# Performance work log

Measured on AMD Instinct MI355X. Metric: run time of the kernel, lower is better.

## Reference

```python
import jax, jax.numpy as jnp
import numpy as np

B, N, D, H, DH = 2, 2048, 1024, 16, 64
INNER = H * DH          # 1024
FF_INNER = 4 * D        # 4096 (GEGLU)
EPS = 1e-5


def setup_inputs() -> dict:
    key = jax.random.key(0)
    ks = jax.random.split(key, 12)
    s = D ** -0.5
    return {
        "x": jax.random.normal(ks[0], (B, N, D), jnp.float32),
        "Wq": jax.random.normal(ks[1], (D, INNER), jnp.float32) * s,
        "Wk": jax.random.normal(ks[2], (D, INNER), jnp.float32) * s,
        "Wv": jax.random.normal(ks[3], (D, INNER), jnp.float32) * s,
        "Wo": jax.random.normal(ks[4], (INNER, D), jnp.float32) * s,
        "bo": jnp.zeros((D,), jnp.float32),
        "ln1_g": jnp.ones((D,), jnp.float32),
        "ln1_b": jnp.zeros((D,), jnp.float32),
        "ln3_g": jnp.ones((D,), jnp.float32),
        "ln3_b": jnp.zeros((D,), jnp.float32),
        "Wff1": jax.random.normal(ks[5], (D, 2 * FF_INNER), jnp.float32) * s,
        "bff1": jnp.zeros((2 * FF_INNER,), jnp.float32),
        "Wff2": jax.random.normal(ks[6], (FF_INNER, D), jnp.float32) * (FF_INNER ** -0.5),
        "bff2": jnp.zeros((D,), jnp.float32),
    }


def _layernorm(x, g, b):
    mu = jnp.mean(x, axis=-1, keepdims=True)
    var = jnp.mean(jnp.square(x - mu), axis=-1, keepdims=True)
    return (x - mu) * jax.lax.rsqrt(var + EPS) * g + b


def reference(x, Wq, Wk, Wv, Wo, bo, ln1_g, ln1_b, ln3_g, ln3_b, Wff1, bff1, Wff2, bff2):
    scale = DH ** -0.5

    # norm1 + self-attention (attn1)
    x_features = _layernorm(x, ln1_g, ln1_b)
    q = (x_features @ Wq).reshape(B, N, H, DH)
    k = (x_features @ Wk).reshape(B, N, H, DH)
    v = (x_features @ Wv).reshape(B, N, H, DH)
    sim = jnp.einsum('bihd,bjhd->bhij', q, k) * scale      # (B,H,N,N) full scores
    attn = jax.nn.softmax(sim, axis=-1)
    inter_out = jnp.einsum('bhij,bjhd->bhid', attn, v)     # (B,H,N,DH)
    out = inter_out.transpose(0, 2, 1, 3).reshape(B, N, INNER)
    attended_x = out @ Wo + bo
    x = attended_x + x

    # norm3 + GEGLU feed-forward
    h = _layernorm(x, ln3_g, ln3_b) @ Wff1 + bff1
    a, gate = h[..., :FF_INNER], h[..., FF_INNER:]
    x = (a * jax.nn.gelu(gate, approximate=False)) @ Wff2 + bff2 + x

    # match torch return: q,k,v as (b h) n d, attn = inter_out (b h n d)
    q_bh = q.transpose(0, 2, 1, 3).reshape(B * H, N, DH)
    k_bh = k.transpose(0, 2, 1, 3).reshape(B * H, N, DH)
    v_bh = v.transpose(0, 2, 1, 3).reshape(B * H, N, DH)
    return (x, q_bh, k_bh, v_bh, inter_out, x_features)
```

## Files before the change

kernel.cpp:

```cpp
#include <hip/hip_runtime.h>
#include <hip/hip_bf16.h>

#define B_ 2
#define N_ 2048
#define D_ 1024
#define H_ 16
#define DH_ 64
#define M_ 4096
#define FFI_ 4096

typedef __attribute__((ext_vector_type(8))) short bh8;
typedef __attribute__((ext_vector_type(4))) float f4;

#define DEV static __device__ __forceinline__

DEV short f2bf(float f) { __hip_bfloat16 h = __float2bfloat16(f); return *reinterpret_cast<short*>(&h); }
DEV float bf2f(short s) { __hip_bfloat16 h = *reinterpret_cast<__hip_bfloat16*>(&s); return __bfloat162float(h); }

#define GLDS(gp, lp) __builtin_amdgcn_global_load_lds((const __attribute__((address_space(1))) void*)(gp), (__attribute__((address_space(3))) void*)(lp), 16, 0, 0)
#define MFMA16(a,b,c) __builtin_amdgcn_mfma_f32_16x16x32_bf16(a,b,c,0,0,0)

__global__ __launch_bounds__(256) void ln_kernel(const float* __restrict__ x,
    const float* __restrict__ g, const float* __restrict__ b,
    float* __restrict__ outF, short* __restrict__ outB)
{
  const int row = blockIdx.x;
  const int t = threadIdx.x;
  const float4 v = reinterpret_cast<const float4*>(x + (long)row*D_)[t];
  float s = v.x+v.y+v.z+v.w;
  float sq = v.x*v.x+v.y*v.y+v.z*v.z+v.w*v.w;
  #pragma unroll
  for (int o=32;o>0;o>>=1){ s += __shfl_xor(s,o); sq += __shfl_xor(sq,o); }
  __shared__ float red[8];
  const int w = t>>6, l = t&63;
  if (l==0){ red[w]=s; red[4+w]=sq; }
  __syncthreads();
  s  = red[0]+red[1]+red[2]+red[3];
  sq = red[4]+red[5]+red[6]+red[7];
  const float mu = s*(1.f/D_);
  const float rstd = rsqrtf(sq*(1.f/D_) - mu*mu + 1e-5f);
  const float4 gv = reinterpret_cast<const float4*>(g)[t];
  const float4 bv = reinterpret_cast<const float4*>(b)[t];
  float4 y;
  y.x=(v.x-mu)*rstd*gv.x+bv.x; y.y=(v.y-mu)*rstd*gv.y+bv.y;
  y.z=(v.z-mu)*rstd*gv.z+bv.z; y.w=(v.w-mu)*rstd*gv.w+bv.w;
  if (outF) reinterpret_cast<float4*>(outF + (long)row*D_)[t] = y;
  short4 ys; ys.x=f2bf(y.x); ys.y=f2bf(y.y); ys.z=f2bf(y.z); ys.w=f2bf(y.w);
  reinterpret_cast<short4*>(outB + (long)row*D_)[t] = ys;
}

__global__ __launch_bounds__(256) void transpose_cast(const float* __restrict__ in,
    short* __restrict__ out, int R, int C)
{
  __shared__ float tile[32][33];
  const int tx = threadIdx.x & 31, ty = threadIdx.x >> 5;
  const int c0 = blockIdx.x*32, r0 = blockIdx.y*32;
  #pragma unroll
  for (int i=0;i<4;i++) tile[ty+i*8][tx] = in[(long)(r0+ty+i*8)*C + c0+tx];
  __syncthreads();
  #pragma unroll
  for (int i=0;i<4;i++) out[(long)(c0+ty+i*8)*R + r0+tx] = f2bf(tile[tx][ty+i*8]);
}

__global__ __launch_bounds__(256) void transpose_cast4(
    const float* __restrict__ i0, const float* __restrict__ i1,
    const float* __restrict__ i2, const float* __restrict__ i3,
    short* __restrict__ o0, short* __restrict__ o1,
    short* __restrict__ o2, short* __restrict__ o3)
{
  const int z = blockIdx.z;
  const float* in = z==0?i0 : z==1?i1 : z==2?i2 : i3;
  short* out      = z==0?o0 : z==1?o1 : z==2?o2 : o3;
  __shared__ float tile[32][33];
  const int tx = threadIdx.x & 31, ty = threadIdx.x >> 5;
  const int c0 = blockIdx.x*32, r0 = blockIdx.y*32;
  #pragma unroll
  for (int i=0;i<4;i++) tile[ty+i*8][tx] = in[(long)(r0+ty+i*8)*1024 + c0+tx];
  __syncthreads();
  #pragma unroll
  for (int i=0;i<4;i++) out[(long)(c0+ty+i*8)*1024 + r0+tx] = f2bf(tile[tx][ty+i*8]);
}

template<int BM>
DEV void gemm_core(const short* __restrict__ A, const short* __restrict__ BT, int K,
                   int m0, int n0, short* lA, short* lB, f4 (&acc)[BM/32][4])
{
  const int t = threadIdx.x, w = t>>6, l = t&63;
  const int wrow = (w>>1)*(BM/2), wcol = (w&1)*64;
  const int lr = l&15, lk = (l>>4)*8;
  const int sr = t>>2, sc = (t&3)*8;
  const short* gA = A  + (long)(m0+sr)*K + sc;
  const short* gB = BT + (long)(n0+sr)*K + sc;
  #pragma unroll
  for (int i=0;i<BM/32;i++)
    #pragma unroll
    for (int j=0;j<4;j++) acc[i][j] = f4{0.f,0.f,0.f,0.f};
  for (int k0=0; k0<K; k0+=32) {
    __syncthreads();
    #pragma unroll
    for (int i=0;i<BM/64;i++)
      GLDS(gA + (long)i*64*K, &lA[i*2048 + w*512]);
    GLDS(gB,              &lB[w*512]);
    GLDS(gB + (long)64*K, &lB[2048 + w*512]);
    gA += 32; gB += 32;
    asm volatile("s_waitcnt vmcnt(0)" ::: "memory");
    __syncthreads();
    bh8 af[BM/32], bf_[4];
    #pragma unroll
    for (int i=0;i<BM/32;i++) af[i] = *reinterpret_cast<const bh8*>(&lA[(wrow+i*16+lr)*32 + lk]);
    #pragma unroll
    for (int j=0;j<4;j++) bf_[j] = *reinterpret_cast<const bh8*>(&lB[(wcol+j*16+lr)*32 + lk]);
    #pragma unroll
    for (int i=0;i<BM/32;i++)
      #pragma unroll
      for (int j=0;j<4;j++)
        acc[i][j] = MFMA16(af[i], bf_[j], acc[i][j]);
  }
}

__global__ __launch_bounds__(256) void gemm_qkv(const short* __restrict__ A,
    const short* __restrict__ BTq, const short* __restrict__ BTk, const short* __restrict__ BTv,
    float* __restrict__ oQ, float* __restrict__ oK, float* __restrict__ oV,
    short* __restrict__ bQ, short* __restrict__ bK, short* __restrict__ bV)
{
  __shared__ short lA[4096], lB[4096];
  const int m0 = blockIdx.x*128;
  const int by = blockIdx.y, sel = by>>3, n0 = (by&7)*128;
  const short* BT = sel==0 ? BTq : (sel==1 ? BTk : BTv);
  float* oF = sel==0 ? oQ : (sel==1 ? oK : oV);
  short* oB = sel==0 ? bQ : (sel==1 ? bK : bV);
  const float bscale = sel==0 ? 0.125f : 1.0f;
  f4 acc[4][4];
  gemm_core<128>(A, BT, 1024, m0, n0, lA, lB, acc);
  const int t = threadIdx.x, w = t>>6, l = t&63;
  const int wrow=(w>>1)*64, wcol=(w&1)*64, lr=l&15;
  #pragma unroll
  for (int i=0;i<4;i++)
    #pragma unroll
    for (int j=0;j<4;j++)
      #pragma unroll
      for (int r=0;r<4;r++) {
        const int grow = m0 + wrow + i*16 + (l>>4)*4 + r;
        const int gcol = n0 + wcol + j*16 + lr;
        const int bb = grow >> 11, nn = grow & 2047;
        const int hh = gcol >> 6, dd = gcol & 63;
        const long oi = ((long)(bb*H_ + hh)*N_ + nn)*DH_ + dd;
        const float v = acc[i][j][r];
        oF[oi] = v;
        oB[oi] = f2bf(v * bscale);
      }
}

template<int MODE, int BM>
__global__ __launch_bounds__(256) void gemm_bt(const short* __restrict__ A,
    const short* __restrict__ BT, int Ndim, int K,
    const float* __restrict__ bias, const float* __restrict__ resid,
    float* __restrict__ outF, short* __restrict__ outB)
{
  __shared__ short lA[BM*32], lB[4096];
  const int m0 = blockIdx.x*BM, n0 = blockIdx.y*128;
  f4 acc[BM/32][4];
  gemm_core<BM>(A, BT, K, m0, n0, lA, lB, acc);
  const int t = threadIdx.x, w=t>>6, l=t&63;
  const int wrow=(w>>1)*(BM/2), wcol=(w&1)*64, lr=l&15;
  #pragma unroll
  for (int i=0;i<BM/32;i++)
    #pragma unroll
    for (int j=0;j<4;j++)
      #pragma unroll
      for (int r=0;r<4;r++) {
        const int grow = m0 + wrow + i*16 + (l>>4)*4 + r;
        const int gcol = n0 + wcol + j*16 + lr;
        const long oi = (long)grow*Ndim + gcol;
        const float v = acc[i][j][r] + bias[gcol];
        if (MODE==1) outF[oi] = v + resid[oi];
        else         outB[oi] = f2bf(v);
      }
}

__global__ __launch_bounds__(256) void attn_kernel(const short* __restrict__ Q,
    const short* __restrict__ Kb, const short* __restrict__ Vb,
    float* __restrict__ interOut, short* __restrict__ attnB)
{
  __shared__ short Kt[2*64*64];
  __shared__ short Vt[2*64*64];
  __shared__ short Pt[4*16*72];
  const int t = threadIdx.x, w = t>>6, l = t&63;
  const int bid = blockIdx.x;
  const int nb = (bid & 7)*128 + (bid >> 3);
  const int bh = nb >> 5;
  const int q0 = (nb & 31)*64;
  const int lr = l&15, lk = (l>>4)*8, g = l>>4;
  const long base = (long)bh * (N_*DH_);
  const int qrow = q0 + w*16;
  bh8 qf0 = *reinterpret_cast<const bh8*>(&Q[base + (long)(qrow+lr)*DH_ + lk]);
  bh8 qf1 = *reinterpret_cast<const bh8*>(&Q[base + (long)(qrow+lr)*DH_ + 32 + lk]);
  f4 o[4];
  #pragma unroll
  for (int i=0;i<4;i++) o[i]=f4{0.f,0.f,0.f,0.f};
  float m_run[4], l_run[4];
  #pragma unroll
  for (int r=0;r<4;r++){ m_run[r]=-1e30f; l_run[r]=0.f; }
  short* Pw = &Pt[w*16*72];
  const char* ldsK = (const char*)Kt;
  const int beta0 = w*2048 + l*16;
  const int srow = t>>3, sdp = t&7, sd = sdp*8;
  const int NT = N_/64;
  int4 vv[2];
  {
    const char* Kg = (const char*)(Kb + base);
    #pragma unroll
    for (int i=0;i<2;i++) {
      const int beta = beta0 + i*1024;
      const int krow = beta>>7, kpch = (beta>>4)&7;
      GLDS(Kg + krow*128 + (kpch ^ (krow&7))*16, (char*)Kt + (w*2+i)*1024);
    }
    #pragma unroll
    for (int it=0; it<2; it++)
      vv[it] = *reinterpret_cast<const int4*>(&Vb[base + (long)(it*32+srow)*DH_ + sd]);
  }
  for (int kt=0; kt<NT; kt++) {
    const int b = kt & 1;
    asm volatile("s_waitcnt vmcnt(0)" ::: "memory");
    #pragma unroll
    for (int it=0; it<2; it++) {
      const short* vs = reinterpret_cast<const short*>(&vv[it]);
      const int cb0 = (it*4 + (srow>>3)) ^ sdp;
      const int jc  = srow & 7;
      #pragma unroll
      for (int e=0;e<8;e++)
        Vt[b*4096 + (sd+e)*64 + ((cb0^e)<<3) + jc] = vs[e];
    }
    if (kt+1 < NT) {
      const char* Kg = (const char*)(Kb + base + (long)(kt+1)*64*DH_);
      #pragma unroll
      for (int i=0;i<2;i++) {
        const int beta = beta0 + i*1024;
        const int krow = beta>>7, kpch = (beta>>4)&7;
        GLDS(Kg + krow*128 + (kpch ^ (krow&7))*16, (char*)Kt + (b^1)*8192 + (w*2+i)*1024);
      }
      #pragma unroll
      for (int it=0; it<2; it++)
        vv[it] = *reinterpret_cast<const int4*>(&Vb[base + (long)((kt+1)*64 + it*32+srow)*DH_ + sd]);
    }
    asm volatile("s_waitcnt lgkmcnt(0)" ::: "memory");
    __builtin_amdgcn_s_barrier();
    f4 s[4];
    __builtin_amdgcn_s_setprio(1);
    #pragma unroll
    for (int cb=0;cb<4;cb++) {
      const int krow = cb*16+lr;
      const char* kr = ldsK + b*8192 + krow*128;
      bh8 kf0 = *reinterpret_cast<const bh8*>(kr + ((g  )^(lr&7))*16);
      bh8 kf1 = *reinterpret_cast<const bh8*>(kr + ((g+4)^(lr&7))*16);
      f4 z = f4{0.f,0.f,0.f,0.f};
      z = MFMA16(qf0, kf0, z);
      z = MFMA16(qf1, kf1, z);
      s[cb] = z;
    }
    __builtin_amdgcn_s_setprio(0);
    float mx[4];
    #pragma unroll
    for (int r=0;r<4;r++) mx[r] = fmaxf(fmaxf(s[0][r],s[1][r]), fmaxf(s[2][r],s[3][r]));
    #pragma unroll
    for (int mk=1; mk<16; mk<<=1)
      #pragma unroll
      for (int r=0;r<4;r++) mx[r] = fmaxf(mx[r], __shfl_xor(mx[r], mk));
    float rs[4];
    #pragma unroll
    for (int r=0;r<4;r++) {
      const float mn = fmaxf(m_run[r], mx[r]);
      const float al = __expf(m_run[r]-mn);
      m_run[r] = mn;
      l_run[r] *= al;
      float sum = 0.f;
      #pragma unroll
      for (int cb=0;cb<4;cb++) {
        const float pv = __expf(s[cb][r]-mn);
        sum += pv;
        Pw[((l>>4)*4 + r)*72 + cb*16 + lr] = f2bf(pv);
      }
      rs[r] = sum;
      #pragma unroll
      for (int cb=0;cb<4;cb++) o[cb][r] *= al;
    }
    #pragma unroll
    for (int mk=1; mk<16; mk<<=1)
      #pragma unroll
      for (int r=0;r<4;r++) rs[r] += __shfl_xor(rs[r], mk);
    #pragma unroll
    for (int r=0;r<4;r++) l_run[r] += rs[r];
    asm volatile("s_waitcnt lgkmcnt(0)" ::: "memory");
    __builtin_amdgcn_sched_barrier(0);
    bh8 pa0 = *reinterpret_cast<const bh8*>(&Pw[lr*72 + lk]);
    bh8 pa1 = *reinterpret_cast<const bh8*>(&Pw[lr*72 + 32 + lk]);
    #pragma unroll
    for (int kk=0; kk<2; kk++) {
      const bh8 pa = kk ? pa1 : pa0;
      __builtin_amdgcn_s_setprio(1);
      #pragma unroll
      for (int db=0; db<4; db++) {
        const int dd = db*16 + lr;
        const int ch = (kk*4 + g) ^ (dd&7) ^ ((dd>>3)&7);
        bh8 vf = *reinterpret_cast<const bh8*>(&Vt[b*4096 + dd*64 + ch*8]);
        o[db] = MFMA16(pa, vf, o[db]);
      }
      __builtin_amdgcn_s_setprio(0);
    }
    __builtin_amdgcn_s_barrier();
  }
  const int bb = bh>>4, hh = bh&15;
  #pragma unroll
  for (int db=0; db<4; db++)
    #pragma unroll
    for (int r=0;r<4;r++) {
      const int n = qrow + (l>>4)*4 + r;
      const int d = db*16 + lr;
      const float v = o[db][r] / l_run[r];
      interOut[base + (long)n*DH_ + d] = v;
      attnB[(long)(bb*N_ + n)*1024 + hh*DH_ + d] = f2bf(v);
    }
}

__global__ __launch_bounds__(256) void gelu_mul(const short* __restrict__ h, short* __restrict__ g)
{
  const long i = ((long)blockIdx.x*256 + threadIdx.x)*8;
  const long m = i >> 12;
  const int j = (int)(i & 4095);
  bh8 av = *reinterpret_cast<const bh8*>(&h[m*8192 + j]);
  bh8 gv = *reinterpret_cast<const bh8*>(&h[m*8192 + 4096 + j]);
  bh8 ov;
  #pragma unroll
  for (int e=0;e<8;e++) {
    const float a  = bf2f(av[e]);
    const float xg = bf2f(gv[e]);
    const float ge = 0.5f*xg*(1.f + erff(xg*0.70710678118f));
    ov[e] = f2bf(a*ge);
  }
  *reinterpret_cast<bh8*>(&g[i]) = ov;
}

extern "C" void kernel_launch(void* const* d_in, const int* in_sizes, int n_in,
                              void* d_out, int out_size, void* d_ws, size_t ws_size,
                              hipStream_t stream)
{
  const float* x    = (const float*)d_in[0];
  const float* Wq   = (const float*)d_in[1];
  const float* Wk   = (const float*)d_in[2];
  const float* Wv   = (const float*)d_in[3];
  const float* Wo   = (const float*)d_in[4];
  const float* bo   = (const float*)d_in[5];
  const float* ln1g = (const float*)d_in[6];
  const float* ln1b = (const float*)d_in[7];
  const float* ln3g = (const float*)d_in[8];
  const float* ln3b = (const float*)d_in[9];
  const float* Wff1 = (const float*)d_in[10];
  const float* bff1 = (const float*)d_in[11];
  const float* Wff2 = (const float*)d_in[12];
  const float* bff2 = (const float*)d_in[13];
  float* out = (float*)d_out;
  const long SZ = (long)M_*D_;
  float* out_x     = out;
  float* out_q     = out + SZ;
  float* out_k     = out + 2*SZ;
  float* out_v     = out + 3*SZ;
  float* out_inter = out + 4*SZ;
  float* out_xf    = out + 5*SZ;

  char* p = (char*)d_ws;
  auto alloc = [&](size_t bytes){ void* r = (void*)p; p += (bytes + 255) & ~(size_t)255; return r; };
  short* xf_bf  = (short*)alloc(SZ*2);
  short* q_bf   = (short*)alloc(SZ*2);
  short* k_bf   = (short*)alloc(SZ*2);
  short* v_bf   = (short*)alloc(SZ*2);
  short* at_bf  = (short*)alloc(SZ*2);
  float* x2     = (float*)alloc(SZ*4);
  short* x2n_bf = (short*)alloc(SZ*2);
  short* h_bf   = (short*)alloc((size_t)M_*8192*2);
  short* g_bf   = (short*)alloc((size_t)M_*4096*2);
  short* WqT    = (short*)alloc((size_t)1024*1024*2);
  short* WkT    = (short*)alloc((size_t)1024*1024*2);
  short* WvT    = (short*)alloc((size_t)1024*1024*2);
  short* WoT    = (short*)alloc((size_t)1024*1024*2);
  short* Wff1T  = (short*)alloc((size_t)8192*1024*2);
  short* Wff2T  = (short*)alloc((size_t)1024*4096*2);
  (void)in_sizes; (void)n_in; (void)out_size; (void)ws_size;

  dim3 blk(256);
  transpose_cast4<<<dim3(32,32,4), blk, 0, stream>>>(Wq, Wk, Wv, Wo, WqT, WkT, WvT, WoT);
  transpose_cast<<<dim3(256,32), blk, 0, stream>>>(Wff1, Wff1T, 1024, 8192);
  transpose_cast<<<dim3(32,128), blk, 0, stream>>>(Wff2, Wff2T, 4096, 1024);
  ln_kernel<<<M_, blk, 0, stream>>>(x, ln1g, ln1b, out_xf, xf_bf);
  gemm_qkv<<<dim3(32,24), blk, 0, stream>>>(xf_bf, WqT, WkT, WvT,
                                            out_q, out_k, out_v, q_bf, k_bf, v_bf);
  attn_kernel<<<1024, blk, 0, stream>>>(q_bf, k_bf, v_bf, out_inter, at_bf);
  gemm_bt<1,64><<<dim3(64,8),  blk, 0, stream>>>(at_bf,  WoT,   1024, 1024, bo,   x,   x2,    nullptr);
  ln_kernel<<<M_, blk, 0, stream>>>(x2, ln3g, ln3b, nullptr, x2n_bf);
  gemm_bt<2,128><<<dim3(32,64), blk, 0, stream>>>(x2n_bf, Wff1T, 8192, 1024, bff1, nullptr, nullptr, h_bf);
  gelu_mul<<<8192, blk, 0, stream>>>(h_bf, g_bf);
  gemm_bt<1,64><<<dim3(64,8),  blk, 0, stream>>>(g_bf,   Wff2T, 1024, 4096, bff2, x2,  out_x, nullptr);
}
```

Before: 605.0 us.

## Double-buffer GEMM core, fuse FF1 with GEGLU, use DPP softmax reductions

The shared GEMM core now double-buffers its LDS tiles, so the next K-slice is prefetched while the current one feeds the MFMAs, and MFMA priority is raised around the math. A new gemm_ff1 kernel computes the value and gate halves of FF1 in the same block and applies GELU and the multiply in its epilogue. This removes the large intermediate h buffer and the separate gelu_mul pass. In attention, the row max and row sum reductions move from shuffles to DPP ops, and V staging drops to a single LDS buffer, which could create a read/write hazard if the synchronisation is not sufficient.

```diff
diff --git a/kernel.cpp b/kernel.cpp
--- a/kernel.cpp
+++ b/kernel.cpp
@@ -16,6 +16,23 @@
 
 DEV short f2bf(float f) { __hip_bfloat16 h = __float2bfloat16(f); return *reinterpret_cast<short*>(&h); }
 DEV float bf2f(short s) { __hip_bfloat16 h = *reinterpret_cast<__hip_bfloat16*>(&s); return __bfloat162float(h); }
+DEV int   f2bits(float f){ int i; __builtin_memcpy(&i,&f,4); return i; }
+DEV float bits2f(int i){ float f; __builtin_memcpy(&f,&i,4); return f; }
+
+DEV float dpp_max16(float x) {
+  x = fmaxf(x, bits2f(__builtin_amdgcn_update_dpp(f2bits(x), f2bits(x), 0xB1, 0xF, 0xF, true)));
+  x = fmaxf(x, bits2f(__builtin_amdgcn_update_dpp(f2bits(x), f2bits(x), 0x4E, 0xF, 0xF, true)));
+  x = fmaxf(x, bits2f(__builtin_amdgcn_update_dpp(f2bits(x), f2bits(x), 0x141,0xF, 0xF, true)));
+  x = fmaxf(x, bits2f(__builtin_amdgcn_update_dpp(f2bits(x), f2bits(x), 0x140,0xF, 0xF, true)));
+  return x;
+}
+DEV float dpp_sum16(float x) {
+  x += bits2f(__builtin_amdgcn_update_dpp(f2bits(x), f2bits(x), 0xB1, 0xF, 0xF, true));
+  x += bits2f(__builtin_amdgcn_update_dpp(f2bits(x), f2bits(x), 0x4E, 0xF, 0xF, true));
+  x += bits2f(__builtin_amdgcn_update_dpp(f2bits(x), f2bits(x), 0x141,0xF, 0xF, true));
+  x += bits2f(__builtin_amdgcn_update_dpp(f2bits(x), f2bits(x), 0x140,0xF, 0xF, true));
+  return x;
+}
 
 #define GLDS(gp, lp) __builtin_amdgcn_global_load_lds((const __attribute__((address_space(1))) void*)(gp), (__attribute__((address_space(3))) void*)(lp), 16, 0, 0)
 #define MFMA16(a,b,c) __builtin_amdgcn_mfma_f32_16x16x32_bf16(a,b,c,0,0,0)
@@ -89,32 +106,46 @@
   const int wrow = (w>>1)*(BM/2), wcol = (w&1)*64;
   const int lr = l&15, lk = (l>>4)*8;
   const int sr = t>>2, sc = (t&3)*8;
+  const int ABUF = BM*32;
   const short* gA = A  + (long)(m0+sr)*K + sc;
   const short* gB = BT + (long)(n0+sr)*K + sc;
   #pragma unroll
   for (int i=0;i<BM/32;i++)
     #pragma unroll
     for (int j=0;j<4;j++) acc[i][j] = f4{0.f,0.f,0.f,0.f};
+  #pragma unroll
+  for (int i=0;i<BM/64;i++) GLDS(gA + (long)i*64*K, &lA[i*2048 + w*512]);
+  GLDS(gB,              &lB[w*512]);
+  GLDS(gB + (long)64*K, &lB[2048 + w*512]);
+  asm volatile("s_waitcnt vmcnt(0)" ::: "memory");
+  __builtin_amdgcn_s_barrier();
+  int cur = 0;
   for (int k0=0; k0<K; k0+=32) {
-    __syncthreads();
-    #pragma unroll
-    for (int i=0;i<BM/64;i++)
-      GLDS(gA + (long)i*64*K, &lA[i*2048 + w*512]);
-    GLDS(gB,              &lB[w*512]);
-    GLDS(gB + (long)64*K, &lB[2048 + w*512]);
-    gA += 32; gB += 32;
-    asm volatile("s_waitcnt vmcnt(0)" ::: "memory");
-    __syncthreads();
+    const short* pA = lA + cur*ABUF;
+    const short* pB = lB + cur*4096;
+    if (k0+32 < K) {
+      const int nb = cur^1;
+      #pragma unroll
+      for (int i=0;i<BM/64;i++) GLDS(gA + 32 + (long)i*64*K, &lA[nb*ABUF + i*2048 + w*512]);
+      GLDS(gB + 32,              &lB[nb*4096 + w*512]);
+      GLDS(gB + 32 + (long)64*K, &lB[nb*4096 + 2048 + w*512]);
+      gA += 32; gB += 32;
+    }
     bh8 af[BM/32], bf_[4];
     #pragma unroll
-    for (int i=0;i<BM/32;i++) af[i] = *reinterpret_cast<const bh8*>(&lA[(wrow+i*16+lr)*32 + lk]);
-    #pragma unroll
-    for (int j=0;j<4;j++) bf_[j] = *reinterpret_cast<const bh8*>(&lB[(wcol+j*16+lr)*32 + lk]);
+    for (int i=0;i<BM/32;i++) af[i] = *reinterpret_cast<const bh8*>(&pA[(wrow+i*16+lr)*32 + lk]);
+    #pragma unroll
+    for (int j=0;j<4;j++) bf_[j] = *reinterpret_cast<const bh8*>(&pB[(wcol+j*16+lr)*32 + lk]);
+    __builtin_amdgcn_s_setprio(1);
     #pragma unroll
     for (int i=0;i<BM/32;i++)
       #pragma unroll
       for (int j=0;j<4;j++)
         acc[i][j] = MFMA16(af[i], bf_[j], acc[i][j]);
+    __builtin_amdgcn_s_setprio(0);
+    asm volatile("s_waitcnt vmcnt(0)" ::: "memory");
+    __builtin_amdgcn_s_barrier();
+    cur ^= 1;
   }
 }
 
@@ -123,7 +154,7 @@
     float* __restrict__ oQ, float* __restrict__ oK, float* __restrict__ oV,
     short* __restrict__ bQ, short* __restrict__ bK, short* __restrict__ bV)
 {
-  __shared__ short lA[4096], lB[4096];
+  __shared__ short lA[2*4096], lB[2*4096];
   const int m0 = blockIdx.x*128;
   const int by = blockIdx.y, sel = by>>3, n0 = (by&7)*128;
   const short* BT = sel==0 ? BTq : (sel==1 ? BTk : BTv);
@@ -157,7 +188,7 @@
     const float* __restrict__ bias, const float* __restrict__ resid,
     float* __restrict__ outF, short* __restrict__ outB)
 {
-  __shared__ short lA[BM*32], lB[4096];
+  __shared__ short lA[2*BM*32], lB[2*4096];
   const int m0 = blockIdx.x*BM, n0 = blockIdx.y*128;
   f4 acc[BM/32][4];
   gemm_core<BM>(A, BT, K, m0, n0, lA, lB, acc);
@@ -178,12 +209,88 @@
       }
 }
 
+__global__ __launch_bounds__(256) void gemm_ff1(const short* __restrict__ A,
+    const short* __restrict__ BT, const float* __restrict__ bias,
+    short* __restrict__ outG)
+{
+  __shared__ short lA[2*2048], lB[2*4096], lC[2*4096];
+  const int m0 = blockIdx.x*64, n0 = blockIdx.y*128;
+  const int t = threadIdx.x, w = t>>6, l = t&63;
+  const int wrow = (w>>1)*32, wcol = (w&1)*64;
+  const int lr = l&15, lk = (l>>4)*8;
+  const int sr = t>>2, sc = (t&3)*8;
+  const int K = 1024;
+  const short* gA = A  + (long)(m0+sr)*K + sc;
+  const short* gB = BT + (long)(n0+sr)*K + sc;
+  const short* gC = BT + (long)(4096+n0+sr)*K + sc;
+  f4 aa[2][4], ag[2][4];
+  #pragma unroll
+  for (int i=0;i<2;i++)
+    #pragma unroll
+    for (int j=0;j<4;j++){ aa[i][j]=f4{0,0,0,0}; ag[i][j]=f4{0,0,0,0}; }
+  GLDS(gA, &lA[w*512]);
+  GLDS(gB,              &lB[w*512]);
+  GLDS(gB + (long)64*K, &lB[2048 + w*512]);
+  GLDS(gC,              &lC[w*512]);
+  GLDS(gC + (long)64*K, &lC[2048 + w*512]);
+  asm volatile("s_waitcnt vmcnt(0)" ::: "memory");
+  __builtin_amdgcn_s_barrier();
+  int cur = 0;
+  for (int k0=0; k0<K; k0+=32) {
+    const short* pA = lA + cur*2048;
+    const short* pB = lB + cur*4096;
+    const short* pC = lC + cur*4096;
+    if (k0+32 < K) {
+      const int nb = cur^1;
+      GLDS(gA + 32, &lA[nb*2048 + w*512]);
+      GLDS(gB + 32,              &lB[nb*4096 + w*512]);
+      GLDS(gB + 32 + (long)64*K, &lB[nb*4096 + 2048 + w*512]);
+      GLDS(gC + 32,              &lC[nb*4096 + w*512]);
+      GLDS(gC + 32 + (long)64*K, &lC[nb*4096 + 2048 + w*512]);
+      gA += 32; gB += 32; gC += 32;
+    }
+    bh8 af[2], bf_[4], cf[4];
+    #pragma unroll
+    for (int i=0;i<2;i++) af[i] = *reinterpret_cast<const bh8*>(&pA[(wrow+i*16+lr)*32 + lk]);
+    #pragma unroll
+    for (int j=0;j<4;j++){
+      bf_[j] = *reinterpret_cast<const bh8*>(&pB[(wcol+j*16+lr)*32 + lk]);
+      cf[j]  = *reinterpret_cast<const bh8*>(&pC[(wcol+j*16+lr)*32 + lk]);
+    }
+    __builtin_amdgcn_s_setprio(1);
+    #pragma unroll
+    for (int i=0;i<2;i++)
+      #pragma unroll
+      for (int j=0;j<4;j++){
+        aa[i][j] = MFMA16(af[i], bf_[j], aa[i][j]);
+        ag[i][j] = MFMA16(af[i], cf[j],  ag[i][j]);
+      }
+    __builtin_amdgcn_s_setprio(0);
+    asm volatile("s_waitcnt vmcnt(0)" ::: "memory");
+    __builtin_amdgcn_s_barrier();
+    cur ^= 1;
+  }
+  #pragma unroll
+  for (int i=0;i<2;i++)
+    #pragma unroll
+    for (int j=0;j<4;j++)
+      #pragma unroll
+      for (int r=0;r<4;r++) {
+        const int grow = m0 + wrow + i*16 + (l>>4)*4 + r;
+        const int gcol = n0 + wcol + j*16 + lr;
+        const float va = aa[i][j][r] + bias[gcol];
+        const float vg = ag[i][j][r] + bias[4096+gcol];
+        const float ge = 0.5f*vg*(1.f + erff(vg*0.70710678118f));
+        outG[(long)grow*4096 + gcol] = f2bf(va*ge);
+      }
+}
+
 __global__ __launch_bounds__(256) void attn_kernel(const short* __restrict__ Q,
     const short* __restrict__ Kb, const short* __restrict__ Vb,
     float* __restrict__ interOut, short* __restrict__ attnB)
 {
   __shared__ short Kt[2*64*64];
-  __shared__ short Vt[2*64*64];
+  __shared__ short Vt[64*64];
   __shared__ short Pt[4*16*72];
   const int t = threadIdx.x, w = t>>6, l = t&63;
   const int bid = blockIdx.x;
@@ -229,7 +336,7 @@
       const int jc  = srow & 7;
       #pragma unroll
       for (int e=0;e<8;e++)
-        Vt[b*4096 + (sd+e)*64 + ((cb0^e)<<3) + jc] = vs[e];
+        Vt[(sd+e)*64 + ((cb0^e)<<3) + jc] = vs[e];
     }
     if (kt+1 < NT) {
       const char* Kg = (const char*)(Kb + base + (long)(kt+1)*64*DH_);
@@ -259,20 +366,13 @@
       s[cb] = z;
     }
     __builtin_amdgcn_s_setprio(0);
-    float mx[4];
-    #pragma unroll
-    for (int r=0;r<4;r++) mx[r] = fmaxf(fmaxf(s[0][r],s[1][r]), fmaxf(s[2][r],s[3][r]));
-    #pragma unroll
-    for (int mk=1; mk<16; mk<<=1)
-      #pragma unroll
-      for (int r=0;r<4;r++) mx[r] = fmaxf(mx[r], __shfl_xor(mx[r], mk));
-    float rs[4];
     #pragma unroll
     for (int r=0;r<4;r++) {
-      const float mn = fmaxf(m_run[r], mx[r]);
+      float mx = fmaxf(fmaxf(s[0][r],s[1][r]), fmaxf(s[2][r],s[3][r]));
+      mx = dpp_max16(mx);
+      const float mn = fmaxf(m_run[r], mx);
       const float al = __expf(m_run[r]-mn);
       m_run[r] = mn;
-      l_run[r] *= al;
       float sum = 0.f;
       #pragma unroll
       for (int cb=0;cb<4;cb++) {
@@ -280,16 +380,10 @@
         sum += pv;
         Pw[((l>>4)*4 + r)*72 + cb*16 + lr] = f2bf(pv);
       }
-      rs[r] = sum;
+      l_run[r] = l_run[r]*al + dpp_sum16(sum);
       #pragma unroll
       for (int cb=0;cb<4;cb++) o[cb][r] *= al;
     }
-    #pragma unroll
-    for (int mk=1; mk<16; mk<<=1)
-      #pragma unroll
-      for (int r=0;r<4;r++) rs[r] += __shfl_xor(rs[r], mk);
-    #pragma unroll
-    for (int r=0;r<4;r++) l_run[r] += rs[r];
     asm volatile("s_waitcnt lgkmcnt(0)" ::: "memory");
     __builtin_amdgcn_sched_barrier(0);
     bh8 pa0 = *reinterpret_cast<const bh8*>(&Pw[lr*72 + lk]);
@@ -302,7 +396,7 @@
       for (int db=0; db<4; db++) {
         const int dd = db*16 + lr;
         const int ch = (kk*4 + g) ^ (dd&7) ^ ((dd>>3)&7);
-        bh8 vf = *reinterpret_cast<const bh8*>(&Vt[b*4096 + dd*64 + ch*8]);
+        bh8 vf = *reinterpret_cast<const bh8*>(&Vt[dd*64 + ch*8]);
         o[db] = MFMA16(pa, vf, o[db]);
       }
       __builtin_amdgcn_s_setprio(0);
@@ -320,24 +414,6 @@
       interOut[base + (long)n*DH_ + d] = v;
       attnB[(long)(bb*N_ + n)*1024 + hh*DH_ + d] = f2bf(v);
     }
-}
-
-__global__ __launch_bounds__(256) void gelu_mul(const short* __restrict__ h, short* __restrict__ g)
-{
-  const long i = ((long)blockIdx.x*256 + threadIdx.x)*8;
-  const long m = i >> 12;
-  const int j = (int)(i & 4095);
-  bh8 av = *reinterpret_cast<const bh8*>(&h[m*8192 + j]);
-  bh8 gv = *reinterpret_cast<const bh8*>(&h[m*8192 + 4096 + j]);
-  bh8 ov;
-  #pragma unroll
-  for (int e=0;e<8;e++) {
-    const float a  = bf2f(av[e]);
-    const float xg = bf2f(gv[e]);
-    const float ge = 0.5f*xg*(1.f + erff(xg*0.70710678118f));
-    ov[e] = f2bf(a*ge);
-  }
-  *reinterpret_cast<bh8*>(&g[i]) = ov;
 }
 
 extern "C" void kernel_launch(void* const* d_in, const int* in_sizes, int n_in,
@@ -376,7 +452,6 @@
   short* at_bf  = (short*)alloc(SZ*2);
   float* x2     = (float*)alloc(SZ*4);
   short* x2n_bf = (short*)alloc(SZ*2);
-  short* h_bf   = (short*)alloc((size_t)M_*8192*2);
   short* g_bf   = (short*)alloc((size_t)M_*4096*2);
   short* WqT    = (short*)alloc((size_t)1024*1024*2);
   short* WkT    = (short*)alloc((size_t)1024*1024*2);
@@ -396,7 +471,6 @@
   attn_kernel<<<1024, blk, 0, stream>>>(q_bf, k_bf, v_bf, out_inter, at_bf);
   gemm_bt<1,64><<<dim3(64,8),  blk, 0, stream>>>(at_bf,  WoT,   1024, 1024, bo,   x,   x2,    nullptr);
   ln_kernel<<<M_, blk, 0, stream>>>(x2, ln3g, ln3b, nullptr, x2n_bf);
-  gemm_bt<2,128><<<dim3(32,64), blk, 0, stream>>>(x2n_bf, Wff1T, 8192, 1024, bff1, nullptr, nullptr, h_bf);
-  gelu_mul<<<8192, blk, 0, stream>>>(h_bf, g_bf);
+  gemm_ff1<<<dim3(64,32), blk, 0, stream>>>(x2n_bf, Wff1T, bff1, g_bf);
   gemm_bt<1,64><<<dim3(64,8),  blk, 0, stream>>>(g_bf,   Wff2T, 1024, 4096, bff2, x2,  out_x, nullptr);
 }
```

Measured after the change: 577.3 us. 1.05x faster.
